# Kernel tuning notes

Measured on AMD Instinct MI355X. Metric: run time of the kernel, lower is better.

## Reference

```python
import jax, jax.numpy as jnp
import numpy as np

BN_EPS = 1e-5


def setup_inputs() -> dict:
    key = jax.random.key(0)
    ks = jax.random.split(key, 16)
    B, n, m, C1, C2 = 8, 8192, 2048, 256, 256
    Cin, H1, H2 = C1 + C2, 512, 512
    inp = {
        'unknown': jax.random.uniform(ks[0], (B, n, 3), jnp.float32),
        'known': jax.random.uniform(ks[1], (B, m, 3), jnp.float32),
        'unknow_feats': jax.random.normal(ks[2], (B, C1, n), jnp.float32),
        'known_feats': jax.random.normal(ks[3], (B, C2, m), jnp.float32),
        # shared-MLP layer 1: Conv2d(512 -> 512, k=1, bias=False) + BN + ReLU
        'W1': jax.random.normal(ks[4], (H1, Cin), jnp.float32) * (1.0 / np.sqrt(Cin)),
        'g1': jax.random.uniform(ks[5], (H1,), jnp.float32, 0.5, 1.5),
        'b1': jax.random.normal(ks[6], (H1,), jnp.float32) * 0.1,
        'm1': jax.random.normal(ks[7], (H1,), jnp.float32) * 0.1,
        'v1': jax.random.uniform(ks[8], (H1,), jnp.float32, 0.5, 1.5),
        # shared-MLP layer 2
        'W2': jax.random.normal(ks[9], (H2, H1), jnp.float32) * (1.0 / np.sqrt(H1)),
        'g2': jax.random.uniform(ks[10], (H2,), jnp.float32, 0.5, 1.5),
        'b2': jax.random.normal(ks[11], (H2,), jnp.float32) * 0.1,
        'm2': jax.random.normal(ks[12], (H2,), jnp.float32) * 0.1,
        'v2': jax.random.uniform(ks[13], (H2,), jnp.float32, 0.5, 1.5),
    }
    return inp


def three_nn(unknown, known):
    # brute-force squared L2 distances (CUDA kernel returns squared dists)
    d2 = jnp.sum((unknown[:, :, None, :] - known[:, None, :, :]) ** 2, axis=-1)  # (B,n,m)
    neg_d, idx = jax.lax.top_k(-d2, 3)  # 3 smallest
    return -neg_d, idx  # (B,n,3), (B,n,3)


def three_interpolate(feats, idx, weight):
    # feats (B,C,m), idx (B,n,3), weight (B,n,3) -> (B,C,n)
    def _one(f, i, w):
        return jnp.einsum('cnk,nk->cn', f[:, i], w)
    return jax.vmap(_one)(feats, idx, weight)


def _conv_bn_relu(x, W, g, b, mu, var):
    # x (B,Cin,n) -> (B,Cout,n); 1x1 conv + inference BatchNorm + ReLU
    y = jnp.einsum('oc,bcn->bon', W, x)
    scale = g / jnp.sqrt(var + BN_EPS)
    y = y * scale[None, :, None] + (b - mu * scale)[None, :, None]
    return jax.nn.relu(y)


def reference(unknown, known, unknow_feats, known_feats,
              W1, g1, b1, m1, v1, W2, g2, b2, m2, v2):
    dist, idx = three_nn(unknown, known)
    dist_recip = 1.0 / (dist + 1e-8)
    weight = dist_recip / jnp.sum(dist_recip, axis=2, keepdims=True)
    new_features = three_interpolate(known_feats, idx, weight)  # (B,C2,n)
    new_features = jnp.concatenate([new_features, unknow_feats], axis=1)  # (B,C1+C2,n)
    h = _conv_bn_relu(new_features, W1, g1, b1, m1, v1)
    out = _conv_bn_relu(h, W2, g2, b2, m2, v2)
    return out  # (B, 512, n)
```

## Files before the change

kernel.cpp:

```cpp
#include <hip/hip_runtime.h>

typedef __bf16 bf16_t;
typedef __bf16 bf16x8 __attribute__((ext_vector_type(8)));
typedef float f32x4 __attribute__((ext_vector_type(4)));

#define AS1 __attribute__((address_space(1)))
#define AS3 __attribute__((address_space(3)))

__device__ __forceinline__ void gload_lds16(const void* g, void* l) {
    __builtin_amdgcn_global_load_lds((const AS1 unsigned int*)g,
                                     (AS3 unsigned int*)l, 16, 0, 0);
}

__device__ __forceinline__ unsigned int pack2(float a, float b) {
    unsigned short lo = __builtin_bit_cast(unsigned short, (bf16_t)a);
    unsigned short hi = __builtin_bit_cast(unsigned short, (bf16_t)b);
    return (unsigned int)lo | ((unsigned int)hi << 16);
}

__global__ __launch_bounds__(256) void conv_w(const float* W, bf16_t* dst) {
    size_t i = (size_t)blockIdx.x * 256 + threadIdx.x;
    dst[i] = (bf16_t)W[i];
}

__global__ __launch_bounds__(512) void bn_prep(
    const float* g1, const float* b1, const float* m1, const float* v1,
    const float* g2, const float* b2, const float* m2, const float* v2,
    float* s1, float* t1, float* s2, float* t2)
{
    int i = threadIdx.x;
    if (i < 512) {
        float s = __fdiv_rn(g1[i], __fsqrt_rn(__fadd_rn(v1[i], 1e-5f)));
        s1[i] = s;
        t1[i] = __fsub_rn(b1[i], __fmul_rn(m1[i], s));
        float q = __fdiv_rn(g2[i], __fsqrt_rn(__fadd_rn(v2[i], 1e-5f)));
        s2[i] = q;
        t2[i] = __fsub_rn(b2[i], __fmul_rn(m2[i], q));
    }
}

__global__ __launch_bounds__(256) void knn3_kernel(
    const float* __restrict__ unknown, const float* __restrict__ known,
    int* __restrict__ idx3, float* __restrict__ w3)
{
    __shared__ float4 kp[2048];
    const int b = blockIdx.y;
    const int tid = threadIdx.x;
    const size_t kb = (size_t)b * 2048 * 3;
    for (int t = tid; t < 2048; t += 256) {
        kp[t] = make_float4(known[kb + t * 3 + 0], known[kb + t * 3 + 1],
                            known[kb + t * 3 + 2], 0.f);
    }
    __syncthreads();

    const int p = blockIdx.x * 256 + tid;
    const size_t qo = ((size_t)b * 8192 + p) * 3;
    const float qx = unknown[qo + 0];
    const float qy = unknown[qo + 1];
    const float qz = unknown[qo + 2];

    float d1 = 1e30f, d2b = 1e30f, d3 = 1e30f;
    int i1 = 0, i2 = 0, i3 = 0;
#pragma unroll 4
    for (int j = 0; j < 2048; ++j) {
        float4 k = kp[j];
        float dx = __fsub_rn(qx, k.x);
        float dy = __fsub_rn(qy, k.y);
        float dz = __fsub_rn(qz, k.z);
        float d = __fadd_rn(__fadd_rn(__fmul_rn(dx, dx), __fmul_rn(dy, dy)),
                            __fmul_rn(dz, dz));
        bool c1 = d < d1, c2 = d < d2b, c3 = d < d3;
        d3 = c2 ? d2b : (c3 ? d : d3);  i3 = c2 ? i2 : (c3 ? j : i3);
        d2b = c1 ? d1 : (c2 ? d : d2b); i2 = c1 ? i1 : (c2 ? j : i2);
        d1 = c1 ? d : d1;               i1 = c1 ? j : i1;
    }
    float r1 = __fdiv_rn(1.f, __fadd_rn(d1, 1e-8f));
    float r2 = __fdiv_rn(1.f, __fadd_rn(d2b, 1e-8f));
    float r3 = __fdiv_rn(1.f, __fadd_rn(d3, 1e-8f));
    float s = __fadd_rn(__fadd_rn(r1, r2), r3);
    const size_t o = ((size_t)b * 8192 + p) * 3;
    idx3[o + 0] = i1; idx3[o + 1] = i2; idx3[o + 2] = i3;
    w3[o + 0] = __fdiv_rn(r1, s);
    w3[o + 1] = __fdiv_rn(r2, s);
    w3[o + 2] = __fdiv_rn(r3, s);
}

__global__ __launch_bounds__(256) void transpose_kf(
    const float* __restrict__ kf, float* __restrict__ kfT)
{
    __shared__ float tile[32][33];
    const int b = blockIdx.z;
    const int m0 = blockIdx.x * 32;
    const int c0 = blockIdx.y * 32;
    const int tx = threadIdx.x & 31;
    const int ty = threadIdx.x >> 5;
#pragma unroll
    for (int k = 0; k < 4; ++k) {
        const int c = c0 + ty + k * 8;
        tile[ty + k * 8][tx] = kf[((size_t)b * 256 + c) * 2048 + m0 + tx];
    }
    __syncthreads();
#pragma unroll
    for (int k = 0; k < 4; ++k) {
        const int m = m0 + ty + k * 8;
        kfT[((size_t)b * 2048 + m) * 256 + c0 + tx] = tile[tx][ty + k * 8];
    }
}

__global__ __launch_bounds__(256) void interp_gather(
    const float* __restrict__ kfT, const int* __restrict__ idx3,
    const float* __restrict__ w3, bf16_t* __restrict__ XT,
    int b0, int p0, int P)
{
    const int bl = blockIdx.y;
    const int bg = b0 + bl;
    const int pt = blockIdx.x * 16 + (threadIdx.x >> 4);
    const int ch = (threadIdx.x & 15) * 16;
    const int p = p0 + pt;

    const size_t ib = ((size_t)bg * 8192 + p) * 3;
    const int i0 = idx3[ib + 0] & 2047;
    const int i1 = idx3[ib + 1] & 2047;
    const int i2 = idx3[ib + 2] & 2047;
    const float w0 = w3[ib + 0], w1 = w3[ib + 1], w2 = w3[ib + 2];

    const float4* r0 = (const float4*)(kfT + ((size_t)bg * 2048 + i0) * 256 + ch);
    const float4* r1 = (const float4*)(kfT + ((size_t)bg * 2048 + i1) * 256 + ch);
    const float4* r2 = (const float4*)(kfT + ((size_t)bg * 2048 + i2) * 256 + ch);

    unsigned int u[8];
#pragma unroll
    for (int q = 0; q < 4; ++q) {
        float4 a = r0[q], bv = r1[q], c = r2[q];
        float v0 = w0 * a.x + w1 * bv.x + w2 * c.x;
        float v1 = w0 * a.y + w1 * bv.y + w2 * c.y;
        float v2 = w0 * a.z + w1 * bv.z + w2 * c.z;
        float v3 = w0 * a.w + w1 * bv.w + w2 * c.w;
        u[q * 2 + 0] = pack2(v0, v1);
        u[q * 2 + 1] = pack2(v2, v3);
    }
    uint4* dst = (uint4*)(XT + ((size_t)bl * P + pt) * 512 + ch);
    dst[0] = make_uint4(u[0], u[1], u[2], u[3]);
    dst[1] = make_uint4(u[4], u[5], u[6], u[7]);
}

__global__ __launch_bounds__(256) void uf_transpose(
    const float* __restrict__ uf, bf16_t* __restrict__ XT,
    int b0, int p0, int P)
{
    __shared__ bf16_t tile[64][66];
    const int bl = blockIdx.z;
    const int bg = b0 + bl;
    const int pc = blockIdx.y * 64;
    const int c0 = blockIdx.x * 64;
    const int tid = threadIdx.x;
    const int pl = tid & 63;
    const int grp = tid >> 6;
    const int p = p0 + pc + pl;

#pragma unroll
    for (int cc = 0; cc < 16; ++cc) {
        const int lc = grp * 16 + cc;
        tile[lc][pl] = (bf16_t)uf[((size_t)bg * 256 + c0 + lc) * 8192 + p];
    }
    __syncthreads();

    const int pr = tid >> 2;
    const int cs = (tid & 3) * 16;
    unsigned int u[8];
#pragma unroll
    for (int q = 0; q < 8; ++q) {
        unsigned short lo = __builtin_bit_cast(unsigned short, tile[cs + 2 * q + 0][pr]);
        unsigned short hi = __builtin_bit_cast(unsigned short, tile[cs + 2 * q + 1][pr]);
        u[q] = (unsigned int)lo | ((unsigned int)hi << 16);
    }
    uint4* dst = (uint4*)(XT + ((size_t)bl * P + pc + pr) * 512 + 256 + c0 + cs);
    dst[0] = make_uint4(u[0], u[1], u[2], u[3]);
    dst[1] = make_uint4(u[4], u[5], u[6], u[7]);
}

template <bool CHAN_IS_M, bool F32_OUT>
__global__ __launch_bounds__(256) void gemm_bt_bn_relu(
    const bf16_t* __restrict__ A, const bf16_t* __restrict__ BT,
    void* __restrict__ Cv,
    const float* __restrict__ scale, const float* __restrict__ shift,
    int ldC, size_t strideA, size_t strideB, size_t strideC, size_t cofs)
{
    __shared__ __align__(16) bf16_t As[128 * 32];
    __shared__ __align__(16) bf16_t Bs[128 * 32];

    const int b = blockIdx.z;
    const int m0 = blockIdx.y * 128;
    const int n0 = blockIdx.x * 128;
    const bf16_t* Ab = A + (size_t)b * strideA + (size_t)m0 * 512;
    const bf16_t* Bb = BT + (size_t)b * strideB + (size_t)n0 * 512;
    const size_t cbase = cofs + (size_t)b * strideC;

    const int tid = threadIdx.x;
    const int lane = tid & 63;
    const int wave = tid >> 6;
    const int wm = (wave & 1) * 64;
    const int wn = (wave >> 1) * 64;

    const int ch0 = tid, ch1 = tid + 256;
    const size_t ga0 = (size_t)(ch0 >> 2) * 512 + (size_t)(ch0 & 3) * 8;
    const size_t ga1 = (size_t)(ch1 >> 2) * 512 + (size_t)(ch1 & 3) * 8;

    const int row_a = lane & 15;
    const int koff = (lane >> 4) * 8;

    f32x4 acc[4][4] = {};

    for (int kt = 0; kt < 512; kt += 32) {
        gload_lds16(Ab + ga0 + kt, As + (size_t)ch0 * 8);
        gload_lds16(Ab + ga1 + kt, As + (size_t)ch1 * 8);
        gload_lds16(Bb + ga0 + kt, Bs + (size_t)ch0 * 8);
        gload_lds16(Bb + ga1 + kt, Bs + (size_t)ch1 * 8);
        __builtin_amdgcn_s_waitcnt(0);
        __syncthreads();

        bf16x8 af[4], bfr[4];
#pragma unroll
        for (int i = 0; i < 4; ++i)
            af[i] = *(const bf16x8*)(As + (size_t)(wm + i * 16 + row_a) * 32 + koff);
#pragma unroll
        for (int j = 0; j < 4; ++j)
            bfr[j] = *(const bf16x8*)(Bs + (size_t)(wn + j * 16 + row_a) * 32 + koff);
#pragma unroll
        for (int i = 0; i < 4; ++i)
#pragma unroll
            for (int j = 0; j < 4; ++j)
                acc[i][j] = __builtin_amdgcn_mfma_f32_16x16x32_bf16(
                    af[i], bfr[j], acc[i][j], 0, 0, 0);
        __syncthreads();
    }

    const int col = lane & 15;
    const int rbase = (lane >> 4) * 4;
#pragma unroll
    for (int i = 0; i < 4; ++i) {
#pragma unroll
        for (int j = 0; j < 4; ++j) {
            const int mb = m0 + wm + i * 16 + rbase;
            const int nn = n0 + wn + j * 16 + col;
            float sc = 0.f, sh = 0.f;
            if (!CHAN_IS_M) { sc = scale[nn]; sh = shift[nn]; }
#pragma unroll
            for (int r = 0; r < 4; ++r) {
                const int mm = mb + r;
                float s = CHAN_IS_M ? scale[mm] : sc;
                float t = CHAN_IS_M ? shift[mm] : sh;
                float v = fmaxf(acc[i][j][r] * s + t, 0.0f);
                const size_t ci = cbase + (size_t)mm * (size_t)ldC + nn;
                if (F32_OUT) ((float*)Cv)[ci] = v;
                else         ((bf16_t*)Cv)[ci] = (bf16_t)v;
            }
        }
    }
}

extern "C" void kernel_launch(void* const* d_in, const int* in_sizes, int n_in,
                              void* d_out, int out_size, void* d_ws, size_t ws_size,
                              hipStream_t stream) {
    (void)in_sizes; (void)n_in; (void)out_size;
    const float* unknown  = (const float*)d_in[0];
    const float* known    = (const float*)d_in[1];
    const float* unknow_f = (const float*)d_in[2];
    const float* known_f  = (const float*)d_in[3];
    const float* W1       = (const float*)d_in[4];
    const float* g1 = (const float*)d_in[5]; const float* b1 = (const float*)d_in[6];
    const float* m1 = (const float*)d_in[7]; const float* v1 = (const float*)d_in[8];
    const float* W2       = (const float*)d_in[9];
    const float* g2 = (const float*)d_in[10]; const float* b2 = (const float*)d_in[11];
    const float* m2 = (const float*)d_in[12]; const float* v2 = (const float*)d_in[13];

    char* ws = (char*)d_ws;
    float* s1 = (float*)(ws + 0);
    float* t1 = s1 + 512;
    float* s2 = s1 + 1024;
    float* t2 = s1 + 1536;
    int*    idx3 = (int*)(ws + 16384);
    float*  w3   = (float*)(ws + 16384 + 786432);
    bf16_t* Wc1  = (bf16_t*)(ws + 1589248);
    bf16_t* Wc2  = (bf16_t*)(ws + 2113536);
    float*  kfT  = (float*)(ws + (3u << 20));
    const size_t FIXED = 20u << 20;

    size_t avail = (ws_size > FIXED) ? (ws_size - FIXED) : 0;
    size_t pts = avail / 2048;
    int nb, P;
    if (pts >= 65536)      { nb = 8; P = 8192; }
    else if (pts >= 8192)  { nb = (int)(pts / 8192); P = 8192; }
    else {
        nb = 1;
        P = (int)((pts / 128) * 128);
        if (P < 128) P = 128;
        if (P > 8192) P = 8192;
    }
    bf16_t* XT = (bf16_t*)(ws + FIXED);
    bf16_t* HT = XT + (size_t)nb * P * 512;

    conv_w<<<1024, 256, 0, stream>>>(W1, Wc1);
    conv_w<<<1024, 256, 0, stream>>>(W2, Wc2);
    bn_prep<<<1, 512, 0, stream>>>(g1, b1, m1, v1, g2, b2, m2, v2, s1, t1, s2, t2);
    knn3_kernel<<<dim3(32, 8), 256, 0, stream>>>(unknown, known, idx3, w3);
    transpose_kf<<<dim3(64, 8, 8), 256, 0, stream>>>(known_f, kfT);

    for (int b0 = 0; b0 < 8; b0 += nb) {
        const int cur = (8 - b0 < nb) ? (8 - b0) : nb;
        for (int p0 = 0; p0 < 8192; p0 += P) {
            const int cp = (8192 - p0 < P) ? (8192 - p0) : P;

            interp_gather<<<dim3(cp / 16, cur), 256, 0, stream>>>(
                kfT, idx3, w3, XT, b0, p0, cp);
            uf_transpose<<<dim3(4, cp / 64, cur), 256, 0, stream>>>(
                unknow_f, XT, b0, p0, cp);

            gemm_bt_bn_relu<false, false><<<dim3(4, cp / 128, cur), 256, 0, stream>>>(
                XT, Wc1, HT, s1, t1, 512,
                (size_t)cp * 512, (size_t)0, (size_t)cp * 512, (size_t)0);

            gemm_bt_bn_relu<true, true><<<dim3(cp / 128, 4, cur), 256, 0, stream>>>(
                Wc2, HT, d_out, s2, t2, 8192,
                (size_t)0, (size_t)cp * 512, (size_t)512 * 8192,
                (size_t)b0 * 512 * 8192 + p0);
        }
    }
}
```

Measured before the change: 464.5 us.

## Split KNN search across waves and interleaved chains, merge top-3 via LDS

The 3-NN kernel used to give each thread one query point and scan all 2048 known points serially, launching only 256 blocks. Now each block covers 64 queries, and its four waves each scan a 512-point slice. Inside a slice each thread keeps four independent top-3 chains, which adds instruction-level parallelism. Partial results are merged in registers and then across waves through shared memory, so four times as many blocks launch. The cost is extra merge work, an LDS round trip and a block barrier, and tie ordering may differ slightly from a serial scan.

```diff
diff --git a/kernel.cpp b/kernel.cpp
--- a/kernel.cpp
+++ b/kernel.cpp
@@ -39,13 +39,26 @@
     }
 }
 
+__device__ __forceinline__ void insdi(float d, int i,
+                                      float& D1, int& I1, float& D2, int& I2,
+                                      float& D3, int& I3) {
+    bool q1 = d < D1, q2 = d < D2, q3 = d < D3;
+    D3 = q2 ? D2 : (q3 ? d : D3);  I3 = q2 ? I2 : (q3 ? i : I3);
+    D2 = q1 ? D1 : (q2 ? d : D2);  I2 = q1 ? I1 : (q2 ? i : I2);
+    D1 = q1 ? d : D1;              I1 = q1 ? i : I1;
+}
+
 __global__ __launch_bounds__(256) void knn3_kernel(
     const float* __restrict__ unknown, const float* __restrict__ known,
     int* __restrict__ idx3, float* __restrict__ w3)
 {
     __shared__ float4 kp[2048];
+    __shared__ float md[4][64][3];
+    __shared__ int   mi[4][64][3];
     const int b = blockIdx.y;
     const int tid = threadIdx.x;
+    const int lane = tid & 63;
+    const int wv = tid >> 6;
     const size_t kb = (size_t)b * 2048 * 3;
     for (int t = tid; t < 2048; t += 256) {
         kp[t] = make_float4(known[kb + t * 3 + 0], known[kb + t * 3 + 1],
@@ -53,36 +66,67 @@
     }
     __syncthreads();
 
-    const int p = blockIdx.x * 256 + tid;
+    const int p = blockIdx.x * 64 + lane;
     const size_t qo = ((size_t)b * 8192 + p) * 3;
     const float qx = unknown[qo + 0];
     const float qy = unknown[qo + 1];
     const float qz = unknown[qo + 2];
 
-    float d1 = 1e30f, d2b = 1e30f, d3 = 1e30f;
-    int i1 = 0, i2 = 0, i3 = 0;
-#pragma unroll 4
-    for (int j = 0; j < 2048; ++j) {
-        float4 k = kp[j];
-        float dx = __fsub_rn(qx, k.x);
-        float dy = __fsub_rn(qy, k.y);
-        float dz = __fsub_rn(qz, k.z);
-        float d = __fadd_rn(__fadd_rn(__fmul_rn(dx, dx), __fmul_rn(dy, dy)),
-                            __fmul_rn(dz, dz));
-        bool c1 = d < d1, c2 = d < d2b, c3 = d < d3;
-        d3 = c2 ? d2b : (c3 ? d : d3);  i3 = c2 ? i2 : (c3 ? j : i3);
-        d2b = c1 ? d1 : (c2 ? d : d2b); i2 = c1 ? i1 : (c2 ? j : i2);
-        d1 = c1 ? d : d1;               i1 = c1 ? j : i1;
-    }
-    float r1 = __fdiv_rn(1.f, __fadd_rn(d1, 1e-8f));
-    float r2 = __fdiv_rn(1.f, __fadd_rn(d2b, 1e-8f));
-    float r3 = __fdiv_rn(1.f, __fadd_rn(d3, 1e-8f));
-    float s = __fadd_rn(__fadd_rn(r1, r2), r3);
-    const size_t o = ((size_t)b * 8192 + p) * 3;
-    idx3[o + 0] = i1; idx3[o + 1] = i2; idx3[o + 2] = i3;
-    w3[o + 0] = __fdiv_rn(r1, s);
-    w3[o + 1] = __fdiv_rn(r2, s);
-    w3[o + 2] = __fdiv_rn(r3, s);
+    float d1[4], d2[4], d3[4];
+    int   i1[4], i2[4], i3[4];
+#pragma unroll
+    for (int c = 0; c < 4; ++c) {
+        d1[c] = 1e30f; d2[c] = 1e30f; d3[c] = 1e30f;
+        i1[c] = 0;     i2[c] = 0;     i3[c] = 0;
+    }
+
+    const int jb = wv * 512;
+#pragma unroll 2
+    for (int t = 0; t < 128; ++t) {
+#pragma unroll
+        for (int c = 0; c < 4; ++c) {
+            const int j = jb + c * 128 + t;
+            float4 k = kp[j];
+            float dx = __fsub_rn(qx, k.x);
+            float dy = __fsub_rn(qy, k.y);
+            float dz = __fsub_rn(qz, k.z);
+            float d = __fadd_rn(__fadd_rn(__fmul_rn(dx, dx), __fmul_rn(dy, dy)),
+                                __fmul_rn(dz, dz));
+            insdi(d, j, d1[c], i1[c], d2[c], i2[c], d3[c], i3[c]);
+        }
+    }
+    float D1 = d1[0], D2 = d2[0], D3 = d3[0];
+    int   I1 = i1[0], I2 = i2[0], I3 = i3[0];
+#pragma unroll
+    for (int c = 1; c < 4; ++c) {
+        insdi(d1[c], i1[c], D1, I1, D2, I2, D3, I3);
+        insdi(d2[c], i2[c], D1, I1, D2, I2, D3, I3);
+        insdi(d3[c], i3[c], D1, I1, D2, I2, D3, I3);
+    }
+    md[wv][lane][0] = D1; md[wv][lane][1] = D2; md[wv][lane][2] = D3;
+    mi[wv][lane][0] = I1; mi[wv][lane][1] = I2; mi[wv][lane][2] = I3;
+    __syncthreads();
+
+    if (tid < 64) {
+        float F1 = md[0][tid][0], F2 = md[0][tid][1], F3 = md[0][tid][2];
+        int   J1 = mi[0][tid][0], J2 = mi[0][tid][1], J3 = mi[0][tid][2];
+#pragma unroll
+        for (int w = 1; w < 4; ++w) {
+            insdi(md[w][tid][0], mi[w][tid][0], F1, J1, F2, J2, F3, J3);
+            insdi(md[w][tid][1], mi[w][tid][1], F1, J1, F2, J2, F3, J3);
+            insdi(md[w][tid][2], mi[w][tid][2], F1, J1, F2, J2, F3, J3);
+        }
+        float r1 = __fdiv_rn(1.f, __fadd_rn(F1, 1e-8f));
+        float r2 = __fdiv_rn(1.f, __fadd_rn(F2, 1e-8f));
+        float r3 = __fdiv_rn(1.f, __fadd_rn(F3, 1e-8f));
+        float s = __fadd_rn(__fadd_rn(r1, r2), r3);
+        const int pp = blockIdx.x * 64 + tid;
+        const size_t o = ((size_t)b * 8192 + pp) * 3;
+        idx3[o + 0] = J1; idx3[o + 1] = J2; idx3[o + 2] = J3;
+        w3[o + 0] = __fdiv_rn(r1, s);
+        w3[o + 1] = __fdiv_rn(r2, s);
+        w3[o + 2] = __fdiv_rn(r3, s);
+    }
 }
 
 __global__ __launch_bounds__(256) void transpose_kf(
@@ -303,7 +347,7 @@
     conv_w<<<1024, 256, 0, stream>>>(W1, Wc1);
     conv_w<<<1024, 256, 0, stream>>>(W2, Wc2);
     bn_prep<<<1, 512, 0, stream>>>(g1, b1, m1, v1, g2, b2, m2, v2, s1, t1, s2, t2);
-    knn3_kernel<<<dim3(32, 8), 256, 0, stream>>>(unknown, known, idx3, w3);
+    knn3_kernel<<<dim3(128, 8), 256, 0, stream>>>(unknown, known, idx3, w3);
     transpose_kf<<<dim3(64, 8, 8), 256, 0, stream>>>(known_f, kfT);
 
     for (int b0 = 0; b0 < 8; b0 += nb) {
```

Result: faster. 431.0 us (-7.2%).
